# Kernel tuning notes

Measured on AMD Instinct MI355X. Metric: run time of the kernel, lower is better.

## Reference

```python
import jax, jax.numpy as jnp
import numpy as np

ROPE_BASE = 10000.0


def _rope_tables(T, d, dtype):
    # inv_freq over even indices, emb = concat(freqs, freqs) -> [T, d]
    inv_freq = 1.0 / (ROPE_BASE ** (jnp.arange(0, d, 2, dtype=jnp.float32) / d))
    t = jnp.arange(T, dtype=jnp.float32)
    freqs = jnp.einsum('i,j->ij', t, inv_freq)          # [T, d/2]
    emb = jnp.concatenate([freqs, freqs], axis=-1)      # [T, d]
    return jnp.cos(emb).astype(dtype), jnp.sin(emb).astype(dtype)


def _rotate_half(x):
    d = x.shape[-1] // 2
    return jnp.concatenate([-x[..., d:], x[..., :d]], axis=-1)


def _apply_rope(x, cos, sin):
    # x: [B, T, H, Dh]; cos/sin: [T, Dh] broadcast over batch and heads
    c = cos[None, :, None, :]
    s = sin[None, :, None, :]
    return x * c + _rotate_half(x) * s


def setup_inputs() -> dict:
    key = jax.random.key(0)
    k1, k2, k3 = jax.random.split(key, 3)
    B, T, C = 2, 2048, 1024
    x = jax.random.normal(k1, (B, T, C), dtype=jnp.float32)
    # weights stored as [in, out] (transposed nn.Linear), scaled like torch init
    W_qkv = jax.random.normal(k2, (C, 3 * C), dtype=jnp.float32) * (C ** -0.5)
    W_proj = jax.random.normal(k3, (C, C), dtype=jnp.float32) * (C ** -0.5)
    return {'x': x, 'W_qkv': W_qkv, 'W_proj': W_proj}


def reference(x, W_qkv, W_proj):
    B, T, C = x.shape
    H = 16
    Dh = C // H
    qkv = x @ W_qkv                                   # [B, T, 3C]
    q, k, v = jnp.split(qkv, 3, axis=-1)
    q = q.reshape(B, T, H, Dh)
    k = k.reshape(B, T, H, Dh)
    v = v.reshape(B, T, H, Dh)
    cos, sin = _rope_tables(T, Dh, x.dtype)
    q = _apply_rope(q, cos, sin)
    k = _apply_rope(k, cos, sin)
    scale = 1.0 / jnp.sqrt(jnp.asarray(Dh, dtype=x.dtype))
    # causal SDPA: scores [B, H, T, T]
    scores = jnp.einsum('bqhd,bkhd->bhqk', q, k) * scale
    causal = jnp.tril(jnp.ones((T, T), dtype=bool))
    scores = jnp.where(causal[None, None], scores, jnp.asarray(-jnp.inf, dtype=scores.dtype))
    attn = jax.nn.softmax(scores, axis=-1)
    y = jnp.einsum('bhqk,bkhd->bqhd', attn, v).reshape(B, T, C)
    return y @ W_proj
```

## Files before the change

### kernel.cpp

```cpp
#include <hip/hip_runtime.h>
#include <cstdint>
#include <cstddef>

typedef __bf16 bf16;
typedef __bf16 bf16x2 __attribute__((ext_vector_type(2)));
typedef __bf16 bf16x4 __attribute__((ext_vector_type(4)));
typedef __bf16 bf16x8 __attribute__((ext_vector_type(8)));
typedef float  f32x4  __attribute__((ext_vector_type(4)));
typedef float  f32x16 __attribute__((ext_vector_type(16)));
typedef int    i32x4  __attribute__((ext_vector_type(4)));

#define G2L(src, dst)                                                          \
  __builtin_amdgcn_global_load_lds(                                            \
      (const __attribute__((address_space(1))) unsigned int*)(src),            \
      (__attribute__((address_space(3))) unsigned int*)(dst), 16, 0, 0)

__global__ void k_f32_to_bf16(const float* __restrict__ in, bf16* __restrict__ out, int n) {
  int i = (blockIdx.x * blockDim.x + threadIdx.x) * 8;
  if (i >= n) return;
  float4 a = *(const float4*)(in + i);
  float4 b = *(const float4*)(in + i + 4);
  bf16x8 o;
  o[0] = (bf16)a.x; o[1] = (bf16)a.y; o[2] = (bf16)a.z; o[3] = (bf16)a.w;
  o[4] = (bf16)b.x; o[5] = (bf16)b.y; o[6] = (bf16)b.z; o[7] = (bf16)b.w;
  *(bf16x8*)(out + i) = o;
}

__global__ void k_transpose_f32_bf16(const float* __restrict__ in, bf16* __restrict__ out,
                                     int R, int C) {
  __shared__ float tile[32][33];
  int c0 = blockIdx.x * 32, r0 = blockIdx.y * 32;
  int tx = threadIdx.x & 31, ty = threadIdx.x >> 5;
#pragma unroll
  for (int i = 0; i < 32; i += 8)
    tile[ty + i][tx] = in[(size_t)(r0 + ty + i) * C + c0 + tx];
  __syncthreads();
#pragma unroll
  for (int i = 0; i < 32; i += 8)
    out[(size_t)(c0 + ty + i) * R + r0 + tx] = (bf16)tile[tx][ty + i];
}

__global__ void k_rope_tables(float* __restrict__ cosT, float* __restrict__ sinT, int total) {
  int i = blockIdx.x * blockDim.x + threadIdx.x;
  if (i >= total) return;
  int t = i >> 5, j = i & 31;
  float inv = powf(10000.0f, -(float)j * (1.0f / 32.0f));
  float f = (float)t * inv;
  cosT[i] = cosf(f);
  sinT[i] = sinf(f);
}

__global__ void k_rope_qk(const bf16* __restrict__ qkv, const float* __restrict__ cosT,
                          const float* __restrict__ sinT, bf16* __restrict__ qr,
                          bf16* __restrict__ kr) {
  int i = blockIdx.x * blockDim.x + threadIdx.x;
  int j = i & 31;
  int h = (i >> 5) & 15;
  int t = (i >> 9) & 2047;
  int b = i >> 20;
  size_t base = (size_t)(b * 2048 + t) * 3072;
  float c = cosT[t * 32 + j], s = sinT[t * 32 + j];
  float qlo = (float)qkv[base + h * 64 + j];
  float qhi = (float)qkv[base + h * 64 + j + 32];
  float klo = (float)qkv[base + 1024 + h * 64 + j];
  float khi = (float)qkv[base + 1024 + h * 64 + j + 32];
  size_t ob = ((size_t)(b * 16 + h) * 2048 + t) * 64;
  const float QS = 0.125f * 1.44269504f;
  qr[ob + j]      = (bf16)((qlo * c - qhi * s) * QS);
  qr[ob + j + 32] = (bf16)((qhi * c + qlo * s) * QS);
  kr[ob + j]      = (bf16)(klo * c - khi * s);
  kr[ob + j + 32] = (bf16)(khi * c + klo * s);
}

__global__ void k_v_scatter(const bf16* __restrict__ qkv, bf16* __restrict__ vt) {
  __shared__ bf16 tile[64][66];
  int bh = blockIdx.y;
  int t0 = blockIdx.x * 64;
  int b = bh >> 4, h = bh & 15;
  int tt = threadIdx.x >> 2, c4 = (threadIdx.x & 3) * 16;
  const bf16* src = qkv + (size_t)(b * 2048 + t0 + tt) * 3072 + 2048 + h * 64 + c4;
  bf16x8 v0 = *(const bf16x8*)src;
  bf16x8 v1 = *(const bf16x8*)(src + 8);
#pragma unroll
  for (int j = 0; j < 8; j++) { tile[tt][c4 + j] = v0[j]; tile[tt][c4 + 8 + j] = v1[j]; }
  __syncthreads();
  int d = threadIdx.x >> 2, tc0 = (threadIdx.x & 3) * 16;
  bf16x8 o0, o1;
#pragma unroll
  for (int j = 0; j < 8; j++) { o0[j] = tile[tc0 + j][d]; o1[j] = tile[tc0 + 8 + j][d]; }
  bf16* dst = vt + ((size_t)bh * 64 + d) * 2048 + t0 + tc0;
  *(bf16x8*)dst = o0;
  *(bf16x8*)(dst + 8) = o1;
}

template <int OUTF32>
__global__ __launch_bounds__(256) void k_gemm_bt(const bf16* __restrict__ A,
                                                 const bf16* __restrict__ Bt,
                                                 float* __restrict__ Cf, bf16* __restrict__ Cb,
                                                 int M, int N, int K) {
  __shared__ __align__(16) bf16 sA[128 * 64];
  __shared__ __align__(16) bf16 sB[128 * 64];
  int nwg = gridDim.x * gridDim.y;
  int idl = blockIdx.y * gridDim.x + blockIdx.x;
  int cpx = nwg >> 3;
  int swz = (idl & 7) * cpx + (idl >> 3);
  int bx = swz % gridDim.x, by = swz / gridDim.x;
  int m0 = by * 128, n0 = bx * 128;
  int t = threadIdx.x, lane = t & 63, w = t >> 6;
  int wr = w >> 1, wc = w & 1;
  int lr = lane & 15, q2 = lane >> 4;
  int srow8 = lane >> 3, pc8 = lane & 7;
  f32x4 acc[4][4] = {};
  for (int k0 = 0; k0 < K; k0 += 64) {
#pragma unroll
    for (int is = 0; is < 4; is++) {
      int r = w * 32 + is * 8 + srow8;
      int lc = pc8 ^ (r & 7);
      G2L(A + (size_t)(m0 + r) * K + k0 + lc * 8, &sA[(w * 32 + is * 8) * 64]);
    }
#pragma unroll
    for (int is = 0; is < 4; is++) {
      int r = w * 32 + is * 8 + srow8;
      int lc = pc8 ^ (r & 7);
      G2L(Bt + (size_t)(n0 + r) * K + k0 + lc * 8, &sB[(w * 32 + is * 8) * 64]);
    }
    __syncthreads();
#pragma unroll
    for (int ch = 0; ch < 2; ch++) {
      bf16x8 af[4], bfr[4];
#pragma unroll
      for (int i = 0; i < 4; i++) {
        int r = wr * 64 + i * 16 + lr;
        af[i] = *(const bf16x8*)&sA[r * 64 + (((ch * 4 + q2) ^ (r & 7)) * 8)];
      }
#pragma unroll
      for (int i = 0; i < 4; i++) {
        int r = wc * 64 + i * 16 + lr;
        bfr[i] = *(const bf16x8*)&sB[r * 64 + (((ch * 4 + q2) ^ (r & 7)) * 8)];
      }
#pragma unroll
      for (int mi = 0; mi < 4; mi++)
#pragma unroll
        for (int ni = 0; ni < 4; ni++)
          acc[mi][ni] = __builtin_amdgcn_mfma_f32_16x16x32_bf16(af[mi], bfr[ni], acc[mi][ni], 0, 0, 0);
    }
    __syncthreads();
  }
  int row_base = m0 + wr * 64, col_base = n0 + wc * 64;
#pragma unroll
  for (int mi = 0; mi < 4; mi++)
#pragma unroll
    for (int ni = 0; ni < 4; ni++) {
      int col = col_base + ni * 16 + lr;
#pragma unroll
      for (int r = 0; r < 4; r++) {
        int row = row_base + mi * 16 + q2 * 4 + r;
        float v = acc[mi][ni][r];
        if (OUTF32) Cf[(size_t)row * N + col] = v;
        else        Cb[(size_t)row * N + col] = (bf16)v;
      }
    }
}

__global__ __launch_bounds__(128) void k_flash_part(const bf16* __restrict__ qr,
                                                    const bf16* __restrict__ kr,
                                                    const bf16* __restrict__ vt,
                                                    bf16* __restrict__ Opart,
                                                    float* __restrict__ ml) {
  const int T = 2048;
  int id = blockIdx.x;
  int slot = id >> 5;
  int bh = id & 31;
  int qt = 31, c = 0;
  {
    int s = slot;
#pragma unroll 1
    for (int q = 31; q >= 0; --q) {
      int n = q / 6 + 1;
      if (s < n) { qt = q; c = s; break; }
      s -= n;
    }
  }
  int kt0 = c * 6;
  int kt1 = qt + 1 < kt0 + 6 ? qt + 1 : kt0 + 6;

  __shared__ __align__(16) bf16 sK[64 * 64];
  __shared__ __align__(16) bf16 sV[64 * 64];
  int t = threadIdx.x, lane = t & 63, w = t >> 6;
  int q31 = lane & 31, hi = lane >> 5;
  int srow8 = lane >> 3, pc8 = lane & 7;

  const bf16* Kbh = kr + (size_t)bh * T * 64;
  const bf16* Vbh = vt + (size_t)bh * 64 * T;

  int qwb = qt * 64 + w * 32;
  int qg = qwb + q31;
  const bf16* qrow = qr + ((size_t)bh * T + qg) * 64 + hi * 8;
  bf16x8 qf[4];
#pragma unroll
  for (int ks = 0; ks < 4; ks++) qf[ks] = *(const bf16x8*)(qrow + ks * 16);
  f32x16 o0 = {}, o1 = {};
  float m = -1e30f, l = 0.f;

  auto stage = [&](int kt) {
#pragma unroll
    for (int is = 0; is < 4; is++) {
      int r = w * 32 + is * 8 + srow8;
      int lc = pc8 ^ (r & 7);
      G2L(Kbh + (size_t)(kt * 64 + r) * 64 + lc * 8, &sK[(w * 32 + is * 8) * 64]);
    }
#pragma unroll
    for (int is = 0; is < 4; is++) {
      int d = w * 32 + is * 8 + srow8;
      int lc = pc8 ^ (d & 7);
      G2L(Vbh + (size_t)d * T + kt * 64 + lc * 8, &sV[(w * 32 + is * 8) * 64]);
    }
  };

  stage(kt0);
  for (int kt = kt0; kt < kt1; kt++) {
    asm volatile("s_waitcnt vmcnt(0)" ::: "memory");
    __builtin_amdgcn_s_barrier();
    asm volatile("" ::: "memory");
    __builtin_amdgcn_sched_barrier(0);
    f32x16 s[2];
    __builtin_amdgcn_s_setprio(1);
#pragma unroll
    for (int kb = 0; kb < 2; kb++) {
      f32x16 a = {};
      int krow = kb * 32 + q31;
#pragma unroll
      for (int ks = 0; ks < 4; ks++) {
        int ch = (ks * 2 + hi) ^ (krow & 7);
        bf16x8 kf = *(const bf16x8*)&sK[krow * 64 + ch * 8];
        a = __builtin_amdgcn_mfma_f32_32x32x16_bf16(kf, qf[ks], a, 0, 0, 0);
      }
      s[kb] = a;
    }
    __builtin_amdgcn_s_setprio(0);
    if (kt == qt) {
      int thr = qg - kt * 64;
#pragma unroll
      for (int kb = 0; kb < 2; kb++)
#pragma unroll
        for (int r = 0; r < 16; r++) {
          int koff = kb * 32 + (r & 3) + 8 * (r >> 2) + 4 * hi;
          if (koff > thr) s[kb][r] = -1e30f;
        }
    }
    float tm[16];
#pragma unroll
    for (int i = 0; i < 16; i++) tm[i] = fmaxf(s[0][i], s[1][i]);
#pragma unroll
    for (int st = 8; st > 0; st >>= 1)
#pragma unroll
      for (int i = 0; i < st; i++) tm[i] = fmaxf(tm[i], tm[i + st]);
    float px = tm[0];
    px = fmaxf(px, __shfl_xor(px, 32, 64));
    if (__builtin_amdgcn_ballot_w64(px > m + 8.f)) {
      float mn = fmaxf(m, px);
      float alpha = exp2f(m - mn);
      m = mn;
#pragma unroll
      for (int r = 0; r < 16; r++) { o0[r] *= alpha; o1[r] *= alpha; }
      l *= alpha;
    }
    float ts[16];
#pragma unroll
    for (int i = 0; i < 16; i++) {
      float p0 = exp2f(s[0][i] - m);
      float p1 = exp2f(s[1][i] - m);
      s[0][i] = p0;
      s[1][i] = p1;
      ts[i] = p0 + p1;
    }
#pragma unroll
    for (int st = 8; st > 0; st >>= 1)
#pragma unroll
      for (int i = 0; i < st; i++) ts[i] += ts[i + st];
    float rs = ts[0];
    rs += __shfl_xor(rs, 32, 64);
    l += rs;
    int pw[4][4];
#pragma unroll
    for (int kb = 0; kb < 2; kb++) {
      int wd[8];
#pragma unroll
      for (int g = 0; g < 4; g++) {
        bf16x2 a, cc;
        a[0] = (bf16)s[kb][4 * g + 0]; a[1] = (bf16)s[kb][4 * g + 1];
        cc[0] = (bf16)s[kb][4 * g + 2]; cc[1] = (bf16)s[kb][4 * g + 3];
        wd[2 * g]     = __builtin_bit_cast(int, a);
        wd[2 * g + 1] = __builtin_bit_cast(int, cc);
      }
      asm volatile("v_permlane32_swap_b32 %0, %1" : "+v"(wd[0]), "+v"(wd[2]));
      asm volatile("v_permlane32_swap_b32 %0, %1" : "+v"(wd[1]), "+v"(wd[3]));
      asm volatile("v_permlane32_swap_b32 %0, %1" : "+v"(wd[4]), "+v"(wd[6]));
      asm volatile("v_permlane32_swap_b32 %0, %1" : "+v"(wd[5]), "+v"(wd[7]));
      pw[2 * kb][0] = wd[0]; pw[2 * kb][1] = wd[1];
      pw[2 * kb][2] = wd[2]; pw[2 * kb][3] = wd[3];
      pw[2 * kb + 1][0] = wd[4]; pw[2 * kb + 1][1] = wd[5];
      pw[2 * kb + 1][2] = wd[6]; pw[2 * kb + 1][3] = wd[7];
    }
    __builtin_amdgcn_s_setprio(1);
#pragma unroll
    for (int ks = 0; ks < 4; ks++) {
      i32x4 pv = {pw[ks][0], pw[ks][1], pw[ks][2], pw[ks][3]};
      bf16x8 pb = __builtin_bit_cast(bf16x8, pv);
      {
        int drow = q31;
        int ch = (ks * 2 + hi) ^ (drow & 7);
        bf16x8 vf = *(const bf16x8*)&sV[drow * 64 + ch * 8];
        o0 = __builtin_amdgcn_mfma_f32_32x32x16_bf16(vf, pb, o0, 0, 0, 0);
      }
      {
        int drow = 32 + q31;
        int ch = (ks * 2 + hi) ^ (drow & 7);
        bf16x8 vf = *(const bf16x8*)&sV[drow * 64 + ch * 8];
        o1 = __builtin_amdgcn_mfma_f32_32x32x16_bf16(vf, pb, o1, 0, 0, 0);
      }
    }
    __builtin_amdgcn_s_setprio(0);
    asm volatile("" ::: "memory");
    __builtin_amdgcn_s_barrier();
    asm volatile("" ::: "memory");
    if (kt + 1 < kt1) stage(kt + 1);
  }
  int qloc = w * 32 + q31;
  bf16* Ob = Opart + (size_t)id * 4096 + qloc * 64;
#pragma unroll
  for (int g = 0; g < 4; g++) {
    bf16x4 v0, v1;
#pragma unroll
    for (int j = 0; j < 4; j++) {
      v0[j] = (bf16)o0[4 * g + j];
      v1[j] = (bf16)o1[4 * g + j];
    }
    *(bf16x4*)&Ob[8 * g + 4 * hi]      = v0;
    *(bf16x4*)&Ob[32 + 8 * g + 4 * hi] = v1;
  }
  if (hi == 0) {
    ml[(size_t)id * 128 + qloc]      = m;
    ml[(size_t)id * 128 + 64 + qloc] = l;
  }
}

__global__ __launch_bounds__(256) void k_combine(const bf16* __restrict__ Opart,
                                                 const float* __restrict__ ml,
                                                 bf16* __restrict__ attn) {
  int bhqt = blockIdx.x;
  int bh = bhqt & 31, qt = bhqt >> 5;
  int b = bh >> 4, h = bh & 15;
  int nch = qt / 6 + 1;
  int slot0 = 0;
#pragma unroll 1
  for (int q = 31; q > qt; --q) slot0 += q / 6 + 1;
  int t = threadIdx.x;
  int q = t >> 2, ds = (t & 3) * 16;
  float M = -1e30f;
  for (int c = 0; c < nch; c++)
    M = fmaxf(M, ml[(size_t)((slot0 + c) * 32 + bh) * 128 + q]);
  float acc[16] = {};
  float L = 0.f;
  for (int c = 0; c < nch; c++) {
    int p = (slot0 + c) * 32 + bh;
    float wgt = exp2f(ml[(size_t)p * 128 + q] - M);
    L += wgt * ml[(size_t)p * 128 + 64 + q];
    const bf16* row = Opart + (size_t)p * 4096 + q * 64 + ds;
    bf16x8 a0 = *(const bf16x8*)row;
    bf16x8 a1 = *(const bf16x8*)(row + 8);
#pragma unroll
    for (int i = 0; i < 8; i++) {
      acc[i]     += wgt * (float)a0[i];
      acc[i + 8] += wgt * (float)a1[i];
    }
  }
  float Linv = 1.0f / L;
  bf16x8 w0, w1;
#pragma unroll
  for (int i = 0; i < 8; i++) {
    w0[i] = (bf16)(acc[i] * Linv);
    w1[i] = (bf16)(acc[i + 8] * Linv);
  }
  bf16* dst = attn + ((size_t)(b * 2048) + qt * 64 + q) * 1024 + h * 64 + ds;
  *(bf16x8*)dst = w0;
  *(bf16x8*)(dst + 8) = w1;
}

extern "C" void kernel_launch(void* const* d_in, const int* in_sizes, int n_in,
                              void* d_out, int out_size, void* d_ws, size_t ws_size,
                              hipStream_t stream) {
  const float* x     = (const float*)d_in[0];
  const float* Wqkv  = (const float*)d_in[1];
  const float* Wproj = (const float*)d_in[2];
  float* outp = (float*)d_out;
  const int B = 2, T = 2048, C = 1024;
  const int M = B * T;

  char* ws = (char*)d_ws;
  size_t off = 0;
  auto alloc = [&](size_t bytes) {
    void* p = ws + off;
    off += (bytes + 255) & ~(size_t)255;
    return p;
  };
  bf16* xb     = (bf16*)alloc((size_t)M * C * 2);
  bf16* wprojt = (bf16*)alloc((size_t)C * C * 2);
  float* cosT  = (float*)alloc((size_t)T * 32 * 4);
  float* sinT  = (float*)alloc((size_t)T * 32 * 4);
  bf16* qkv    = (bf16*)alloc((size_t)M * 3 * C * 2);
  bf16* wqkvt  = (bf16*)alloc((size_t)3 * C * C * 2);
  bf16* qr     = (bf16*)alloc((size_t)M * C * 2);
  bf16* kr     = (bf16*)alloc((size_t)M * C * 2);
  bf16* vt     = (bf16*)alloc((size_t)M * C * 2);
  bf16* attn   = xb;
  bf16* Opart  = qkv;
  float* ml    = (float*)(qkv + (size_t)3264 * 4096);

  k_f32_to_bf16<<<dim3(M * C / 8 / 256), dim3(256), 0, stream>>>(x, xb, M * C);
  k_transpose_f32_bf16<<<dim3(3 * C / 32, C / 32), dim3(256), 0, stream>>>(Wqkv, wqkvt, C, 3 * C);
  k_transpose_f32_bf16<<<dim3(C / 32, C / 32), dim3(256), 0, stream>>>(Wproj, wprojt, C, C);
  k_rope_tables<<<dim3(T * 32 / 256), dim3(256), 0, stream>>>(cosT, sinT, T * 32);
  k_gemm_bt<0><<<dim3(3 * C / 128, M / 128), dim3(256), 0, stream>>>(xb, wqkvt, (float*)nullptr, qkv, M, 3 * C, C);
  k_rope_qk<<<dim3((B * T * 16 * 32) / 256), dim3(256), 0, stream>>>(qkv, cosT, sinT, qr, kr);
  k_v_scatter<<<dim3(T / 64, 32), dim3(256), 0, stream>>>(qkv, vt);
  k_flash_part<<<dim3(3264), dim3(128), 0, stream>>>(qr, kr, vt, Opart, ml);
  k_combine<<<dim3(1024), dim3(256), 0, stream>>>(Opart, ml, attn);
  k_gemm_bt<1><<<dim3(C / 128, M / 128), dim3(256), 0, stream>>>(attn, wprojt, outp, (bf16*)nullptr, M, C, C);
}
```

Baseline: 142.9 us.

## Fuse RoPE with V transpose and streamline flash softmax with raw exp2

Merges the RoPE kernel and the V scatter/transpose kernel into one launch that reads each qkv row with vectorized 16-byte loads and writes Q/K with vector stores, removing a launch and the scalar, poorly coalesced accesses. In the flash kernel, the conditional lazy rescale is replaced by an unconditional rescale folded into l and the output accumulators. exp2f is swapped for raw v_exp_f32 inline asm, and the max reduction uses three-operand max chains. The unconditional rescale adds 32 multiplies per tile but removes the ballot branch. Raw v_exp_f32 drops the library's denormal and range handling.

```diff
diff --git a/kernel.cpp b/kernel.cpp
--- a/kernel.cpp
+++ b/kernel.cpp
@@ -9,6 +9,15 @@
 typedef float  f32x4  __attribute__((ext_vector_type(4)));
 typedef float  f32x16 __attribute__((ext_vector_type(16)));
 typedef int    i32x4  __attribute__((ext_vector_type(4)));
+
+__device__ __forceinline__ float fexp2(float x) {
+  float r;
+  asm("v_exp_f32 %0, %1" : "=v"(r) : "v"(x));
+  return r;
+}
+__device__ __forceinline__ float m3(float a, float b, float c) {
+  return fmaxf(fmaxf(a, b), c);
+}
 
 #define G2L(src, dst)                                                          \
   __builtin_amdgcn_global_load_lds(                                            \
@@ -50,39 +59,45 @@
   sinT[i] = sinf(f);
 }
 
-__global__ void k_rope_qk(const bf16* __restrict__ qkv, const float* __restrict__ cosT,
-                          const float* __restrict__ sinT, bf16* __restrict__ qr,
-                          bf16* __restrict__ kr) {
-  int i = blockIdx.x * blockDim.x + threadIdx.x;
-  int j = i & 31;
-  int h = (i >> 5) & 15;
-  int t = (i >> 9) & 2047;
-  int b = i >> 20;
-  size_t base = (size_t)(b * 2048 + t) * 3072;
-  float c = cosT[t * 32 + j], s = sinT[t * 32 + j];
-  float qlo = (float)qkv[base + h * 64 + j];
-  float qhi = (float)qkv[base + h * 64 + j + 32];
-  float klo = (float)qkv[base + 1024 + h * 64 + j];
-  float khi = (float)qkv[base + 1024 + h * 64 + j + 32];
-  size_t ob = ((size_t)(b * 16 + h) * 2048 + t) * 64;
-  const float QS = 0.125f * 1.44269504f;
-  qr[ob + j]      = (bf16)((qlo * c - qhi * s) * QS);
-  qr[ob + j + 32] = (bf16)((qhi * c + qlo * s) * QS);
-  kr[ob + j]      = (bf16)(klo * c - khi * s);
-  kr[ob + j + 32] = (bf16)(khi * c + klo * s);
-}
-
-__global__ void k_v_scatter(const bf16* __restrict__ qkv, bf16* __restrict__ vt) {
+__global__ __launch_bounds__(256) void k_rope_v(const bf16* __restrict__ qkv,
+                                                const float* __restrict__ cosT,
+                                                const float* __restrict__ sinT,
+                                                bf16* __restrict__ qr,
+                                                bf16* __restrict__ kr,
+                                                bf16* __restrict__ vt) {
   __shared__ bf16 tile[64][66];
   int bh = blockIdx.y;
   int t0 = blockIdx.x * 64;
   int b = bh >> 4, h = bh & 15;
-  int tt = threadIdx.x >> 2, c4 = (threadIdx.x & 3) * 16;
-  const bf16* src = qkv + (size_t)(b * 2048 + t0 + tt) * 3072 + 2048 + h * 64 + c4;
-  bf16x8 v0 = *(const bf16x8*)src;
-  bf16x8 v1 = *(const bf16x8*)(src + 8);
+  int tt = threadIdx.x >> 2, g = threadIdx.x & 3;
+  int c4 = g * 16;
+  const bf16* row = qkv + (size_t)(b * 2048 + t0 + tt) * 3072 + h * 64;
+  bf16x8 v0 = *(const bf16x8*)(row + 2048 + c4);
+  bf16x8 v1 = *(const bf16x8*)(row + 2048 + c4 + 8);
 #pragma unroll
   for (int j = 0; j < 8; j++) { tile[tt][c4 + j] = v0[j]; tile[tt][c4 + 8 + j] = v1[j]; }
+  int tglob = t0 + tt;
+  size_t ob = ((size_t)bh * 2048 + tglob) * 64;
+  const float QS = 0.125f * 1.44269504f;
+  bf16x8 qlo = *(const bf16x8*)(row + g * 8);
+  bf16x8 qhi = *(const bf16x8*)(row + 32 + g * 8);
+  bf16x8 klo = *(const bf16x8*)(row + 1024 + g * 8);
+  bf16x8 khi = *(const bf16x8*)(row + 1024 + 32 + g * 8);
+  bf16x8 qo0, qo1, ko0, ko1;
+#pragma unroll
+  for (int j = 0; j < 8; j++) {
+    float c = cosT[tglob * 32 + g * 8 + j], s = sinT[tglob * 32 + g * 8 + j];
+    float ql = (float)qlo[j], qh = (float)qhi[j];
+    float kl = (float)klo[j], kh = (float)khi[j];
+    qo0[j] = (bf16)((ql * c - qh * s) * QS);
+    qo1[j] = (bf16)((qh * c + ql * s) * QS);
+    ko0[j] = (bf16)(kl * c - kh * s);
+    ko1[j] = (bf16)(kh * c + kl * s);
+  }
+  *(bf16x8*)&qr[ob + g * 8]      = qo0;
+  *(bf16x8*)&qr[ob + 32 + g * 8] = qo1;
+  *(bf16x8*)&kr[ob + g * 8]      = ko0;
+  *(bf16x8*)&kr[ob + 32 + g * 8] = ko1;
   __syncthreads();
   int d = threadIdx.x >> 2, tc0 = (threadIdx.x & 3) * 16;
   bf16x8 o0, o1;
@@ -251,25 +266,23 @@
     float tm[16];
 #pragma unroll
     for (int i = 0; i < 16; i++) tm[i] = fmaxf(s[0][i], s[1][i]);
-#pragma unroll
-    for (int st = 8; st > 0; st >>= 1)
-#pragma unroll
-      for (int i = 0; i < st; i++) tm[i] = fmaxf(tm[i], tm[i + st]);
-    float px = tm[0];
+    float a0 = m3(tm[0], tm[1], tm[2]);
+    float a1 = m3(tm[3], tm[4], tm[5]);
+    float a2 = m3(tm[6], tm[7], tm[8]);
+    float a3 = m3(tm[9], tm[10], tm[11]);
+    float a4 = m3(tm[12], tm[13], tm[14]);
+    float b0 = m3(a0, a1, tm[15]);
+    float b1 = m3(a2, a3, a4);
+    float px = fmaxf(b0, b1);
     px = fmaxf(px, __shfl_xor(px, 32, 64));
-    if (__builtin_amdgcn_ballot_w64(px > m + 8.f)) {
-      float mn = fmaxf(m, px);
-      float alpha = exp2f(m - mn);
-      m = mn;
-#pragma unroll
-      for (int r = 0; r < 16; r++) { o0[r] *= alpha; o1[r] *= alpha; }
-      l *= alpha;
-    }
+    float mn = fmaxf(m, px);
+    float alpha = fexp2(m - mn);
+    m = mn;
     float ts[16];
 #pragma unroll
     for (int i = 0; i < 16; i++) {
-      float p0 = exp2f(s[0][i] - m);
-      float p1 = exp2f(s[1][i] - m);
+      float p0 = fexp2(s[0][i] - m);
+      float p1 = fexp2(s[1][i] - m);
       s[0][i] = p0;
       s[1][i] = p1;
       ts[i] = p0 + p1;
@@ -280,7 +293,7 @@
       for (int i = 0; i < st; i++) ts[i] += ts[i + st];
     float rs = ts[0];
     rs += __shfl_xor(rs, 32, 64);
-    l += rs;
+    l = l * alpha + rs;
     int pw[4][4];
 #pragma unroll
     for (int kb = 0; kb < 2; kb++) {
@@ -302,6 +315,8 @@
       pw[2 * kb + 1][0] = wd[4]; pw[2 * kb + 1][1] = wd[5];
       pw[2 * kb + 1][2] = wd[6]; pw[2 * kb + 1][3] = wd[7];
     }
+#pragma unroll
+    for (int r = 0; r < 16; r++) { o0[r] *= alpha; o1[r] *= alpha; }
     __builtin_amdgcn_s_setprio(1);
 #pragma unroll
     for (int ks = 0; ks < 4; ks++) {
@@ -364,7 +379,7 @@
   float L = 0.f;
   for (int c = 0; c < nch; c++) {
     int p = (slot0 + c) * 32 + bh;
-    float wgt = exp2f(ml[(size_t)p * 128 + q] - M);
+    float wgt = fexp2(ml[(size_t)p * 128 + q] - M);
     L += wgt * ml[(size_t)p * 128 + 64 + q];
     const bf16* row = Opart + (size_t)p * 4096 + q * 64 + ds;
     bf16x8 a0 = *(const bf16x8*)row;
@@ -422,8 +437,7 @@
   k_transpose_f32_bf16<<<dim3(C / 32, C / 32), dim3(256), 0, stream>>>(Wproj, wprojt, C, C);
   k_rope_tables<<<dim3(T * 32 / 256), dim3(256), 0, stream>>>(cosT, sinT, T * 32);
   k_gemm_bt<0><<<dim3(3 * C / 128, M / 128), dim3(256), 0, stream>>>(xb, wqkvt, (float*)nullptr, qkv, M, 3 * C, C);
-  k_rope_qk<<<dim3((B * T * 16 * 32) / 256), dim3(256), 0, stream>>>(qkv, cosT, sinT, qr, kr);
-  k_v_scatter<<<dim3(T / 64, 32), dim3(256), 0, stream>>>(qkv, vt);
+  k_rope_v<<<dim3(T / 64, 32), dim3(256), 0, stream>>>(qkv, cosT, sinT, qr, kr, vt);
   k_flash_part<<<dim3(3264), dim3(128), 0, stream>>>(qr, kr, vt, Opart, ml);
   k_combine<<<dim3(1024), dim3(256), 0, stream>>>(Opart, ml, attn);
   k_gemm_bt<1><<<dim3(C / 128, M / 128), dim3(256), 0, stream>>>(attn, wprojt, outp, (bf16*)nullptr, M, C, C);
```

New measurement: 130.8 us. -8.5%, faster.
